# Optimization experiments

Measured on AMD Instinct MI355X. Metric: run time of the kernel, lower is better.

## Reference

```python
import jax, jax.numpy as jnp
import numpy as np

N_NODES = 50000
N_EDGES = 800000
F_IN = 64
F_HID = 64
K = 3


def _cheb_norm(edge_index, edge_weight, n):
    # PyG ChebConv sym normalization with lambda_max=2: Lhat = -D^{-1/2} A D^{-1/2}
    # (diagonal of Lhat is exactly 0, so self-loop terms vanish)
    row, col = edge_index[0], edge_index[1]
    deg = jax.ops.segment_sum(edge_weight, row, num_segments=n)
    dis = jnp.where(deg > 0, jax.lax.rsqrt(jnp.where(deg > 0, deg, 1.0)), 0.0)
    return -dis[row] * edge_weight * dis[col]


def _prop(x, row, col, norm, n):
    # out[i] = sum_{e: col[e]=i} norm[e] * x[row[e]]
    return jax.ops.segment_sum(x[row] * norm[:, None], col, num_segments=n)


def _cheb_conv(x, W, b, row, col, norm, n):
    # ChebConv K=3: Tx0=x, Tx1=Lhat x, Tx2=2 Lhat Tx1 - Tx0
    tx0 = x
    tx1 = _prop(x, row, col, norm, n)
    tx2 = 2.0 * _prop(tx1, row, col, norm, n) - tx0
    return tx0 @ W[0] + tx1 @ W[1] + tx2 @ W[2] + b


def setup_inputs() -> dict:
    key = jax.random.key(0)
    ks = jax.random.split(key, 20)
    inp = {
        "x": jax.random.normal(ks[0], (N_NODES, F_IN), dtype=jnp.float32),
        "edge_index": jax.random.randint(ks[1], (2, N_EDGES), 0, N_NODES, dtype=jnp.int32),
        "edge_weight": jax.random.uniform(ks[2], (N_EDGES,), dtype=jnp.float32),
    }
    # 6 ChebConvs: x->gate (F_IN->F_HID) and h->gate (F_HID->F_HID) for z, r, h
    names_in = [("Wxz", "bxz", F_IN), ("Whz", "bhz", F_HID), ("Wxr", "bxr", F_IN),
                ("Whr", "bhr", F_HID), ("Wxh", "bxh", F_IN), ("Whh", "bhh", F_HID)]
    for i, (wn, bn, fin) in enumerate(names_in):
        scale = 1.0 / np.sqrt(fin)
        inp[wn] = jax.random.normal(ks[3 + i], (K, fin, F_HID), dtype=jnp.float32) * scale
        inp[bn] = jnp.zeros((F_HID,), dtype=jnp.float32)
    inp["Wlin"] = jax.random.normal(ks[12], (F_HID, 2), dtype=jnp.float32) * (1.0 / np.sqrt(F_HID))
    inp["blin"] = jnp.zeros((2,), dtype=jnp.float32)
    return inp


def reference(x, edge_index, edge_weight, Wxz, bxz, Whz, bhz, Wxr, bxr, Whr, bhr,
              Wxh, bxh, Whh, bhh, Wlin, blin):
    n = x.shape[0]
    row, col = edge_index[0], edge_index[1]
    norm = _cheb_norm(edge_index, edge_weight, n)
    h0 = jnp.zeros((n, F_HID), dtype=x.dtype)
    # GConvGRU single step (initial hidden state = 0)
    z = jax.nn.sigmoid(_cheb_conv(x, Wxz, bxz, row, col, norm, n)
                       + _cheb_conv(h0, Whz, bhz, row, col, norm, n))
    r = jax.nn.sigmoid(_cheb_conv(x, Wxr, bxr, row, col, norm, n)
                       + _cheb_conv(h0, Whr, bhr, row, col, norm, n))
    h_tilde = jnp.tanh(_cheb_conv(x, Wxh, bxh, row, col, norm, n)
                       + _cheb_conv(h0 * r, Whh, bhh, row, col, norm, n))
    h = z * h0 + (1.0 - z) * h_tilde
    # head: dropout in eval mode (identity) -> tanh -> linear -> sigmoid
    return jax.nn.sigmoid(jnp.tanh(h) @ Wlin + blin)
```

## Files before the change

### kernel.cpp

```cpp
#include <hip/hip_runtime.h>
#include <hip/hip_bf16.h>

#define N_NODES 50000
#define N_EDGES 800000
#define NB1 400
#define CH  2000
#define NBKT 196
#define CAP 8192
#define SORT_MAX 6144

typedef unsigned short ushort_t;
typedef unsigned long long u64;
typedef __attribute__((ext_vector_type(8))) short bf16x8;
typedef __attribute__((ext_vector_type(4))) float f32x4;

constexpr int GCUR_O  = 0;
constexpr int DIS_O   = 512;
constexpr int OFF_O   = 50512;
constexpr int CSLOT_O = 100544;
constexpr int RSLOT_O = 3311808;
constexpr int RW_O    = 4917440;
constexpr int ABUF_O  = 6517440;
constexpr int PBUF_O  = 11317440;
constexpr int XS_O    = 11329728;
constexpr int T1S_O   = RSLOT_O;

__device__ __forceinline__ ushort_t f32_to_bf16(float f) {
    unsigned u = __float_as_uint(f);
    u += 0x7fffu + ((u >> 16) & 1u);
    return (ushort_t)(u >> 16);
}
__device__ __forceinline__ float bflo(unsigned u) { return __uint_as_float(u << 16); }
__device__ __forceinline__ float bfhi(unsigned u) { return __uint_as_float(u & 0xffff0000u); }
__device__ __forceinline__ unsigned packbf2(float a, float b) {
    return (unsigned)f32_to_bf16(a) | ((unsigned)f32_to_bf16(b) << 16);
}
__device__ __forceinline__ float fsigmoid(float x) { return 1.f / (1.f + __expf(-x)); }
__device__ __forceinline__ float ftanh(float x) {
    x = fminf(15.f, fmaxf(-15.f, x));
    float e = __expf(2.f * x);
    return (e - 1.f) / (e + 1.f);
}

__global__ __launch_bounds__(512) void k1(
    const int* __restrict__ ei, const float* __restrict__ ew,
    const float* __restrict__ x, const float* __restrict__ Wxz,
    const float* __restrict__ Wxh, unsigned* __restrict__ gcur,
    u64* __restrict__ cslot, unsigned* __restrict__ rslot,
    unsigned* __restrict__ abuf, ushort_t* __restrict__ pbuf) {
    int bid = blockIdx.x, t = threadIdx.x;
    if (bid < NB1) {
        __shared__ unsigned colbuf[CH], rowbuf[CH];
        __shared__ unsigned hc[256], hr[256], bc[256], br[256];
        if (t < 256) { hc[t] = 0; hr[t] = 0; }
        __syncthreads();
        int e0 = bid * CH;
        for (int i = t; i < CH; i += 512) {
            unsigned r = (unsigned)ei[e0 + i];
            unsigned c = (unsigned)ei[N_EDGES + e0 + i];
            rowbuf[i] = r;
            colbuf[i] = c;
            atomicAdd(&hc[c >> 8], 1u);
            atomicAdd(&hr[r >> 8], 1u);
        }
        __syncthreads();
        if (t < NBKT) {
            bc[t] = atomicAdd(&gcur[t], hc[t]);
            br[t] = atomicAdd(&gcur[256 + t], hr[t]);
        }
        __syncthreads();
        if (t < 256) { hc[t] = 0; hr[t] = 0; }
        __syncthreads();
        for (int i = t; i < CH; i += 512) {
            unsigned c = colbuf[i];
            unsigned r = rowbuf[i];
            unsigned w = __float_as_uint(ew[e0 + i]);
            unsigned dc = c >> 8;
            unsigned pc = bc[dc] + atomicAdd(&hc[dc], 1u);
            if (pc < CAP)
                cslot[dc * CAP + pc] = ((u64)w << 32) | ((c & 255u) << 16) | (r & 0xFFFFu);
            unsigned dr = r >> 8;
            unsigned pr = br[dr] + atomicAdd(&hr[dr], 1u);
            if (pr < CAP) rslot[dr * CAP + pr] = (w & 0xFFFFFF00u) | (r & 255u);
        }
    } else if (bid < NB1 + 98) {
        int n0 = (bid - NB1) * 512;
        for (int idx = t; idx < 512 * 32; idx += 512) {
            int n = n0 + (idx >> 5);
            if (n < N_NODES) {
                int q = idx & 31;
                float2 xv = ((const float2*)x)[n * 32 + q];
                abuf[n * 96 + q] = packbf2(xv.x, xv.y);
            }
        }
    } else {
        for (int idx = t; idx < 24576; idx += 512) {
            int k = idx >> 7, n = idx & 127;
            float v = (n < 64) ? Wxz[k * 64 + n] : Wxh[k * 64 + (n - 64)];
            int c = n >> 4, s = k >> 5, l = (((k >> 3) & 3) << 4) | (n & 15), j = k & 7;
            pbuf[((c * 6 + s) * 64 + l) * 8 + j] = f32_to_bf16(v);
        }
    }
}

__global__ __launch_bounds__(512) void k2(
    const float* __restrict__ x, const unsigned* __restrict__ gcur,
    const u64* __restrict__ cslot, const unsigned* __restrict__ rslot,
    float* __restrict__ dis, int* __restrict__ off,
    u64* __restrict__ rw, unsigned* __restrict__ xs) {
    int bid = blockIdx.x, t = threadIdx.x;
    __shared__ unsigned rawA[SORT_MAX], rawB[SORT_MAX];
    __shared__ unsigned hist[256], hsc[256], cur[256], gs[256];
    __shared__ float facc[256];

    if (bid < NBKT) {
        if (t < 256) {
            gs[t] = (t < NBKT) ? gcur[t] : 0u;
            hist[t] = 0;
        }
        __syncthreads();
        for (int o = 1; o < 256; o <<= 1) {
            unsigned v = (t < 256 && t >= o) ? gs[t - o] : 0u;
            __syncthreads();
            if (t < 256) gs[t] += v;
            __syncthreads();
        }
        unsigned szb = gcur[bid];
        unsigned sz = min(szb, (unsigned)SORT_MAX);
        unsigned base = gs[bid] - szb;
        for (unsigned i = t; i < sz; i += 512) {
            u64 v = cslot[bid * CAP + i];
            unsigned lo = (unsigned)v;
            rawA[i] = lo;
            rawB[i] = (unsigned)(v >> 32);
            atomicAdd(&hist[(lo >> 16) & 255u], 1u);
        }
        __syncthreads();
        unsigned h0 = (t < 256) ? hist[t] : 0u;
        if (t < 256) hsc[t] = h0;
        __syncthreads();
        for (int o = 1; o < 256; o <<= 1) {
            unsigned v = (t < 256 && t >= o) ? hsc[t - o] : 0u;
            __syncthreads();
            if (t < 256) hsc[t] += v;
            __syncthreads();
        }
        if (t < 256) {
            hsc[t] -= h0;
            cur[t] = 0u;
            int c = bid * 256 + t;
            if (c <= N_NODES) off[c] = (int)(base + hsc[t]);
        }
        __syncthreads();
        for (unsigned i = t; i < sz; i += 512) {
            unsigned lo = rawA[i];
            unsigned d = (lo >> 16) & 255u;
            unsigned p = hsc[d] + atomicAdd(&cur[d], 1u);
            rw[base + p] = ((u64)rawB[i] << 32) | (lo & 0xFFFFu);
        }
    } else {
        int b = bid - NBKT;
        if (t < 256) facc[t] = 0.f;
        __syncthreads();
        unsigned szr = min(gcur[256 + b], (unsigned)CAP);
        for (unsigned i = t; i < szr; i += 512) {
            unsigned v = rslot[b * CAP + i];
            atomicAdd(&facc[v & 255u], __uint_as_float(v & 0xFFFFFF00u));
        }
        __syncthreads();
        if (t < 256) {
            float d = facc[t];
            float r = d > 0.f ? rsqrtf(d) : 0.f;
            facc[t] = r;
            int n = b * 256 + t;
            if (n < N_NODES) dis[n] = r;
        }
        __syncthreads();
        for (int idx = t; idx < 8192; idx += 512) {
            int nl = idx >> 5, q = idx & 31;
            int n = b * 256 + nl;
            if (n < N_NODES) {
                float2 xv = ((const float2*)x)[n * 32 + q];
                float r = facc[nl];
                xs[n * 32 + q] = packbf2(r * xv.x, r * xv.y);
            }
        }
    }
}

__global__ __launch_bounds__(256) void k_prop(
    const int* __restrict__ off, const u64* __restrict__ rw,
    const unsigned* __restrict__ xsrc, const float* __restrict__ dis,
    const float* __restrict__ xf, unsigned* __restrict__ abuf,
    unsigned* __restrict__ t1s, int mode) {
    int node = (blockIdx.x * 256 + threadIdx.x) >> 6;
    if (node >= N_NODES) return;
    int lane = threadIdx.x & 63, h = lane >> 5, q = lane & 31;
    int b = off[node], end = off[node + 1];
    float di = dis[node];
    float acc0 = 0.f, acc1 = 0.f;
    for (; b + 7 < end; b += 8) {
        u64 v0 = rw[b + h], v1 = rw[b + h + 2], v2 = rw[b + h + 4], v3 = rw[b + h + 6];
        unsigned r0 = (unsigned)v0 & 0xFFFFu, r1 = (unsigned)v1 & 0xFFFFu;
        unsigned r2 = (unsigned)v2 & 0xFFFFu, r3 = (unsigned)v3 & 0xFFFFu;
        float a0 = __uint_as_float((unsigned)(v0 >> 32));
        float a1 = __uint_as_float((unsigned)(v1 >> 32));
        float a2 = __uint_as_float((unsigned)(v2 >> 32));
        float a3 = __uint_as_float((unsigned)(v3 >> 32));
        unsigned u0 = xsrc[r0 * 32 + q], u1 = xsrc[r1 * 32 + q];
        unsigned u2 = xsrc[r2 * 32 + q], u3 = xsrc[r3 * 32 + q];
        acc0 += a0 * bflo(u0) + a1 * bflo(u1) + a2 * bflo(u2) + a3 * bflo(u3);
        acc1 += a0 * bfhi(u0) + a1 * bfhi(u1) + a2 * bfhi(u2) + a3 * bfhi(u3);
    }
    for (; b + 1 < end; b += 2) {
        u64 v = rw[b + h];
        unsigned r = (unsigned)v & 0xFFFFu;
        float a = __uint_as_float((unsigned)(v >> 32));
        unsigned u = xsrc[r * 32 + q];
        acc0 += a * bflo(u); acc1 += a * bfhi(u);
    }
    if (b < end && h == 0) {
        u64 v = rw[b];
        unsigned r = (unsigned)v & 0xFFFFu;
        float a = __uint_as_float((unsigned)(v >> 32));
        unsigned u = xsrc[r * 32 + q];
        acc0 += a * bflo(u); acc1 += a * bfhi(u);
    }
    acc0 += __shfl_xor(acc0, 32, 64);
    acc1 += __shfl_xor(acc1, 32, 64);
    if (h == 0) {
        float t0 = -di * acc0, t1v = -di * acc1;
        if (mode == 0) {
            abuf[node * 96 + 32 + q] = packbf2(t0, t1v);
            t1s[node * 32 + q] = packbf2(di * t0, di * t1v);
        } else {
            float2 xv = ((const float2*)xf)[node * 32 + q];
            abuf[node * 96 + 64 + q] = packbf2(2.f * t0 - xv.x, 2.f * t1v - xv.y);
        }
    }
}

__global__ __launch_bounds__(256) void k_gemm(
    const ushort_t* __restrict__ ab, const ushort_t* __restrict__ pbuf,
    const float* __restrict__ bxz, const float* __restrict__ bhz,
    const float* __restrict__ bxh, const float* __restrict__ bhh,
    const float* __restrict__ Wlin, const float* __restrict__ blin,
    float2* __restrict__ out) {
    __shared__ ushort_t bsh[24576];
    int tid = threadIdx.x;
    {
        uint4* s4 = (uint4*)bsh;
        const uint4* g4 = (const uint4*)pbuf;
        for (int i = tid; i < 3072; i += 256) s4[i] = g4[i];
    }
    __syncthreads();

    int wave = tid >> 6, lane = tid & 63;
    int quad = lane >> 4, m = lane & 15;
    int arow = blockIdx.x * 64 + wave * 16 + m;
    const ushort_t* ap = ab + (size_t)arow * 192 + quad * 8;

    f32x4 acc[8];
#pragma unroll
    for (int c = 0; c < 8; ++c) acc[c] = (f32x4){0.f, 0.f, 0.f, 0.f};
#pragma unroll
    for (int s = 0; s < 6; ++s) {
        bf16x8 af = *(const bf16x8*)(ap + s * 32);
#pragma unroll
        for (int c = 0; c < 8; ++c) {
            bf16x8 bfr = *(const bf16x8*)(bsh + ((c * 6 + s) * 64 + lane) * 8);
            acc[c] = __builtin_amdgcn_mfma_f32_16x16x32_bf16(af, bfr, acc[c], 0, 0, 0);
        }
    }
    float bzv[4], bhv[4], wl0[4], wl1[4];
#pragma unroll
    for (int c = 0; c < 4; ++c) {
        int col = c * 16 + m;
        bzv[c] = bxz[col] + bhz[col];
        bhv[c] = bxh[col] + bhh[col];
        wl0[c] = Wlin[2 * col];
        wl1[c] = Wlin[2 * col + 1];
    }
    float bl0 = blin[0], bl1 = blin[1];
#pragma unroll
    for (int i = 0; i < 4; ++i) {
        float p0 = 0.f, p1 = 0.f;
#pragma unroll
        for (int c = 0; c < 4; ++c) {
            float z  = fsigmoid(acc[c][i] + bzv[c]);
            float ht = ftanh(acc[c + 4][i] + bhv[c]);
            float t  = ftanh((1.f - z) * ht);
            p0 += t * wl0[c];
            p1 += t * wl1[c];
        }
        for (int o = 1; o <= 8; o <<= 1) {
            p0 += __shfl_xor(p0, o, 64);
            p1 += __shfl_xor(p1, o, 64);
        }
        int g = blockIdx.x * 64 + wave * 16 + quad * 4 + i;
        if (m == 0 && g < N_NODES)
            out[g] = make_float2(fsigmoid(p0 + bl0), fsigmoid(p1 + bl1));
    }
}

extern "C" void kernel_launch(void* const* d_in, const int* in_sizes, int n_in,
                              void* d_out, int out_size, void* d_ws, size_t ws_size,
                              hipStream_t stream) {
    const float* x    = (const float*)d_in[0];
    const int*   ei   = (const int*)d_in[1];
    const float* ew   = (const float*)d_in[2];
    const float* Wxz  = (const float*)d_in[3];
    const float* bxz  = (const float*)d_in[4];
    const float* bhz  = (const float*)d_in[6];
    const float* Wxh  = (const float*)d_in[11];
    const float* bxh  = (const float*)d_in[12];
    const float* bhh  = (const float*)d_in[14];
    const float* Wlin = (const float*)d_in[15];
    const float* blin = (const float*)d_in[16];

    float*    ws    = (float*)d_ws;
    unsigned* gcur  = (unsigned*)(ws + GCUR_O);
    float*    dis   = ws + DIS_O;
    int*      off   = (int*)(ws + OFF_O);
    u64*      cslot = (u64*)(ws + CSLOT_O);
    unsigned* rslot = (unsigned*)(ws + RSLOT_O);
    u64*      rw    = (u64*)(ws + RW_O);
    unsigned* abuf  = (unsigned*)(ws + ABUF_O);
    ushort_t* pbuf  = (ushort_t*)(ws + PBUF_O);
    unsigned* xs    = (unsigned*)(ws + XS_O);
    unsigned* t1s   = (unsigned*)(ws + T1S_O);

    hipMemsetAsync(d_ws, 0, 512 * 4, stream);

    k1<<<NB1 + 98 + 1, 512, 0, stream>>>(ei, ew, x, Wxz, Wxh, gcur, cslot, rslot, abuf, pbuf);
    k2<<<NBKT * 2, 512, 0, stream>>>(x, gcur, cslot, rslot, dis, off, rw, xs);
    k_prop<<<12500, 256, 0, stream>>>(off, rw, xs, dis, x, abuf, t1s, 0);
    k_prop<<<12500, 256, 0, stream>>>(off, rw, t1s, dis, x, abuf, abuf, 1);
    k_gemm<<<782, 256, 0, stream>>>((const ushort_t*)abuf, pbuf, bxz, bhz, bxh, bhh,
                                    Wlin, blin, (float2*)d_out);
}
```

Before: 214.2 us.

## Fuse graph build, normalization and both propagations into one cooperative kernel

```diff
diff --git a/kernel.cpp b/kernel.cpp
--- a/kernel.cpp
+++ b/kernel.cpp
@@ -1,5 +1,7 @@
 #include <hip/hip_runtime.h>
 #include <hip/hip_bf16.h>
+#include <hip/hip_cooperative_groups.h>
+namespace cg = cooperative_groups;
 
 #define N_NODES 50000
 #define N_EDGES 800000
@@ -7,7 +9,7 @@
 #define CH  2000
 #define NBKT 196
 #define CAP 8192
-#define SORT_MAX 6144
+#define GRID_ALL 512
 
 typedef unsigned short ushort_t;
 typedef unsigned long long u64;
@@ -42,17 +44,25 @@
     return (e - 1.f) / (e + 1.f);
 }
 
-__global__ __launch_bounds__(512) void k1(
+__global__ __launch_bounds__(512, 4) void k_all(
     const int* __restrict__ ei, const float* __restrict__ ew,
     const float* __restrict__ x, const float* __restrict__ Wxz,
     const float* __restrict__ Wxh, unsigned* __restrict__ gcur,
     u64* __restrict__ cslot, unsigned* __restrict__ rslot,
-    unsigned* __restrict__ abuf, ushort_t* __restrict__ pbuf) {
-    int bid = blockIdx.x, t = threadIdx.x;
+    float* __restrict__ dis, int* __restrict__ off, u64* __restrict__ rw,
+    unsigned* __restrict__ abuf, ushort_t* __restrict__ pbuf,
+    unsigned* __restrict__ xs, unsigned* __restrict__ t1s) {
+    cg::grid_group grid = cg::this_grid();
+    const int bid = blockIdx.x, t = threadIdx.x;
+    __shared__ unsigned colbuf[CH], rowbuf[CH];
+    __shared__ unsigned h1[256], h2[256], b1[256], b2[256];
+    __shared__ float facc[256];
+
+    if (bid == 0) gcur[t] = 0u;
+    grid.sync();
+
     if (bid < NB1) {
-        __shared__ unsigned colbuf[CH], rowbuf[CH];
-        __shared__ unsigned hc[256], hr[256], bc[256], br[256];
-        if (t < 256) { hc[t] = 0; hr[t] = 0; }
+        if (t < 256) { h1[t] = 0; h2[t] = 0; }
         __syncthreads();
         int e0 = bid * CH;
         for (int i = t; i < CH; i += 512) {
@@ -60,27 +70,27 @@
             unsigned c = (unsigned)ei[N_EDGES + e0 + i];
             rowbuf[i] = r;
             colbuf[i] = c;
-            atomicAdd(&hc[c >> 8], 1u);
-            atomicAdd(&hr[r >> 8], 1u);
+            atomicAdd(&h1[c >> 8], 1u);
+            atomicAdd(&h2[r >> 8], 1u);
         }
         __syncthreads();
         if (t < NBKT) {
-            bc[t] = atomicAdd(&gcur[t], hc[t]);
-            br[t] = atomicAdd(&gcur[256 + t], hr[t]);
-        }
-        __syncthreads();
-        if (t < 256) { hc[t] = 0; hr[t] = 0; }
+            b1[t] = atomicAdd(&gcur[t], h1[t]);
+            b2[t] = atomicAdd(&gcur[256 + t], h2[t]);
+        }
+        __syncthreads();
+        if (t < 256) { h1[t] = 0; h2[t] = 0; }
         __syncthreads();
         for (int i = t; i < CH; i += 512) {
             unsigned c = colbuf[i];
             unsigned r = rowbuf[i];
             unsigned w = __float_as_uint(ew[e0 + i]);
             unsigned dc = c >> 8;
-            unsigned pc = bc[dc] + atomicAdd(&hc[dc], 1u);
+            unsigned pc = b1[dc] + atomicAdd(&h1[dc], 1u);
             if (pc < CAP)
                 cslot[dc * CAP + pc] = ((u64)w << 32) | ((c & 255u) << 16) | (r & 0xFFFFu);
             unsigned dr = r >> 8;
-            unsigned pr = br[dr] + atomicAdd(&hr[dr], 1u);
+            unsigned pr = b2[dr] + atomicAdd(&h2[dr], 1u);
             if (pr < CAP) rslot[dr * CAP + pr] = (w & 0xFFFFFF00u) | (r & 255u);
         }
     } else if (bid < NB1 + 98) {
@@ -93,7 +103,7 @@
                 abuf[n * 96 + q] = packbf2(xv.x, xv.y);
             }
         }
-    } else {
+    } else if (bid == NB1 + 98) {
         for (int idx = t; idx < 24576; idx += 512) {
             int k = idx >> 7, n = idx & 127;
             float v = (n < 64) ? Wxz[k * 64 + n] : Wxh[k * 64 + (n - 64)];
@@ -101,72 +111,58 @@
             pbuf[((c * 6 + s) * 64 + l) * 8 + j] = f32_to_bf16(v);
         }
     }
-}
-
-__global__ __launch_bounds__(512) void k2(
-    const float* __restrict__ x, const unsigned* __restrict__ gcur,
-    const u64* __restrict__ cslot, const unsigned* __restrict__ rslot,
-    float* __restrict__ dis, int* __restrict__ off,
-    u64* __restrict__ rw, unsigned* __restrict__ xs) {
-    int bid = blockIdx.x, t = threadIdx.x;
-    __shared__ unsigned rawA[SORT_MAX], rawB[SORT_MAX];
-    __shared__ unsigned hist[256], hsc[256], cur[256], gs[256];
-    __shared__ float facc[256];
+    grid.sync();
 
     if (bid < NBKT) {
         if (t < 256) {
-            gs[t] = (t < NBKT) ? gcur[t] : 0u;
-            hist[t] = 0;
+            b1[t] = (t < NBKT) ? gcur[t] : 0u;
+            h1[t] = 0;
         }
         __syncthreads();
         for (int o = 1; o < 256; o <<= 1) {
-            unsigned v = (t < 256 && t >= o) ? gs[t - o] : 0u;
+            unsigned v = (t < 256 && t >= o) ? b1[t - o] : 0u;
             __syncthreads();
-            if (t < 256) gs[t] += v;
+            if (t < 256) b1[t] += v;
             __syncthreads();
         }
         unsigned szb = gcur[bid];
-        unsigned sz = min(szb, (unsigned)SORT_MAX);
-        unsigned base = gs[bid] - szb;
+        unsigned sz = min(szb, (unsigned)CAP);
+        unsigned base = b1[bid] - szb;
+        const u64* cs = cslot + (size_t)bid * CAP;
+        for (unsigned i = t; i < sz; i += 512)
+            atomicAdd(&h1[((unsigned)cs[i] >> 16) & 255u], 1u);
+        __syncthreads();
+        unsigned h0 = (t < 256) ? h1[t] : 0u;
+        if (t < 256) h2[t] = h0;
+        __syncthreads();
+        for (int o = 1; o < 256; o <<= 1) {
+            unsigned v = (t < 256 && t >= o) ? h2[t - o] : 0u;
+            __syncthreads();
+            if (t < 256) h2[t] += v;
+            __syncthreads();
+        }
+        if (t < 256) {
+            h2[t] -= h0;
+            b2[t] = 0u;
+            int c = bid * 256 + t;
+            if (c <= N_NODES) off[c] = (int)(base + h2[t]);
+        }
+        __syncthreads();
         for (unsigned i = t; i < sz; i += 512) {
-            u64 v = cslot[bid * CAP + i];
+            u64 v = cs[i];
             unsigned lo = (unsigned)v;
-            rawA[i] = lo;
-            rawB[i] = (unsigned)(v >> 32);
-            atomicAdd(&hist[(lo >> 16) & 255u], 1u);
-        }
-        __syncthreads();
-        unsigned h0 = (t < 256) ? hist[t] : 0u;
-        if (t < 256) hsc[t] = h0;
-        __syncthreads();
-        for (int o = 1; o < 256; o <<= 1) {
-            unsigned v = (t < 256 && t >= o) ? hsc[t - o] : 0u;
-            __syncthreads();
-            if (t < 256) hsc[t] += v;
-            __syncthreads();
-        }
-        if (t < 256) {
-            hsc[t] -= h0;
-            cur[t] = 0u;
-            int c = bid * 256 + t;
-            if (c <= N_NODES) off[c] = (int)(base + hsc[t]);
-        }
-        __syncthreads();
-        for (unsigned i = t; i < sz; i += 512) {
-            unsigned lo = rawA[i];
             unsigned d = (lo >> 16) & 255u;
-            unsigned p = hsc[d] + atomicAdd(&cur[d], 1u);
-            rw[base + p] = ((u64)rawB[i] << 32) | (lo & 0xFFFFu);
-        }
-    } else {
+            unsigned p = h2[d] + atomicAdd(&b2[d], 1u);
+            rw[base + p] = ((v >> 32) << 32) | (lo & 0xFFFFu);
+        }
+    } else if (bid < 2 * NBKT) {
         int b = bid - NBKT;
         if (t < 256) facc[t] = 0.f;
         __syncthreads();
         unsigned szr = min(gcur[256 + b], (unsigned)CAP);
-        for (unsigned i = t; i < szr; i += 512) {
-            unsigned v = rslot[b * CAP + i];
-            atomicAdd(&facc[v & 255u], __uint_as_float(v & 0xFFFFFF00u));
-        }
+        const unsigned* rs = rslot + (size_t)b * CAP;
+        for (unsigned i = t; i < szr; i += 512)
+            atomicAdd(&facc[rs[i] & 255u], __uint_as_float(rs[i] & 0xFFFFFF00u));
         __syncthreads();
         if (t < 256) {
             float d = facc[t];
@@ -186,56 +182,70 @@
             }
         }
     }
-}
-
-__global__ __launch_bounds__(256) void k_prop(
-    const int* __restrict__ off, const u64* __restrict__ rw,
-    const unsigned* __restrict__ xsrc, const float* __restrict__ dis,
-    const float* __restrict__ xf, unsigned* __restrict__ abuf,
-    unsigned* __restrict__ t1s, int mode) {
-    int node = (blockIdx.x * 256 + threadIdx.x) >> 6;
-    if (node >= N_NODES) return;
-    int lane = threadIdx.x & 63, h = lane >> 5, q = lane & 31;
-    int b = off[node], end = off[node + 1];
-    float di = dis[node];
-    float acc0 = 0.f, acc1 = 0.f;
-    for (; b + 7 < end; b += 8) {
-        u64 v0 = rw[b + h], v1 = rw[b + h + 2], v2 = rw[b + h + 4], v3 = rw[b + h + 6];
-        unsigned r0 = (unsigned)v0 & 0xFFFFu, r1 = (unsigned)v1 & 0xFFFFu;
-        unsigned r2 = (unsigned)v2 & 0xFFFFu, r3 = (unsigned)v3 & 0xFFFFu;
-        float a0 = __uint_as_float((unsigned)(v0 >> 32));
-        float a1 = __uint_as_float((unsigned)(v1 >> 32));
-        float a2 = __uint_as_float((unsigned)(v2 >> 32));
-        float a3 = __uint_as_float((unsigned)(v3 >> 32));
-        unsigned u0 = xsrc[r0 * 32 + q], u1 = xsrc[r1 * 32 + q];
-        unsigned u2 = xsrc[r2 * 32 + q], u3 = xsrc[r3 * 32 + q];
-        acc0 += a0 * bflo(u0) + a1 * bflo(u1) + a2 * bflo(u2) + a3 * bflo(u3);
-        acc1 += a0 * bfhi(u0) + a1 * bfhi(u1) + a2 * bfhi(u2) + a3 * bfhi(u3);
-    }
-    for (; b + 1 < end; b += 2) {
-        u64 v = rw[b + h];
-        unsigned r = (unsigned)v & 0xFFFFu;
-        float a = __uint_as_float((unsigned)(v >> 32));
-        unsigned u = xsrc[r * 32 + q];
-        acc0 += a * bflo(u); acc1 += a * bfhi(u);
-    }
-    if (b < end && h == 0) {
-        u64 v = rw[b];
-        unsigned r = (unsigned)v & 0xFFFFu;
-        float a = __uint_as_float((unsigned)(v >> 32));
-        unsigned u = xsrc[r * 32 + q];
-        acc0 += a * bflo(u); acc1 += a * bfhi(u);
-    }
-    acc0 += __shfl_xor(acc0, 32, 64);
-    acc1 += __shfl_xor(acc1, 32, 64);
-    if (h == 0) {
-        float t0 = -di * acc0, t1v = -di * acc1;
-        if (mode == 0) {
+    grid.sync();
+
+    {
+        int hw = (bid * 512 + t) >> 5, q = t & 31;
+        for (int node = hw; node < N_NODES; node += GRID_ALL * 16) {
+            int b = off[node], end = off[node + 1];
+            float di = dis[node];
+            float a0 = 0.f, a1 = 0.f;
+            for (; b + 3 < end; b += 4) {
+                u64 v0 = rw[b], v1 = rw[b + 1], v2 = rw[b + 2], v3 = rw[b + 3];
+                unsigned u0 = xs[((unsigned)v0 & 0xFFFFu) * 32 + q];
+                unsigned u1 = xs[((unsigned)v1 & 0xFFFFu) * 32 + q];
+                unsigned u2 = xs[((unsigned)v2 & 0xFFFFu) * 32 + q];
+                unsigned u3 = xs[((unsigned)v3 & 0xFFFFu) * 32 + q];
+                float w0 = __uint_as_float((unsigned)(v0 >> 32));
+                float w1 = __uint_as_float((unsigned)(v1 >> 32));
+                float w2 = __uint_as_float((unsigned)(v2 >> 32));
+                float w3 = __uint_as_float((unsigned)(v3 >> 32));
+                a0 += w0 * bflo(u0) + w1 * bflo(u1) + w2 * bflo(u2) + w3 * bflo(u3);
+                a1 += w0 * bfhi(u0) + w1 * bfhi(u1) + w2 * bfhi(u2) + w3 * bfhi(u3);
+            }
+            for (; b < end; ++b) {
+                u64 v = rw[b];
+                unsigned u = xs[((unsigned)v & 0xFFFFu) * 32 + q];
+                float w = __uint_as_float((unsigned)(v >> 32));
+                a0 += w * bflo(u);
+                a1 += w * bfhi(u);
+            }
+            float t0 = -di * a0, t1v = -di * a1;
             abuf[node * 96 + 32 + q] = packbf2(t0, t1v);
             t1s[node * 32 + q] = packbf2(di * t0, di * t1v);
-        } else {
-            float2 xv = ((const float2*)xf)[node * 32 + q];
-            abuf[node * 96 + 64 + q] = packbf2(2.f * t0 - xv.x, 2.f * t1v - xv.y);
+        }
+    }
+    grid.sync();
+
+    {
+        int hw = (bid * 512 + t) >> 5, q = t & 31;
+        for (int node = hw; node < N_NODES; node += GRID_ALL * 16) {
+            int b = off[node], end = off[node + 1];
+            float di = dis[node];
+            float a0 = 0.f, a1 = 0.f;
+            for (; b + 3 < end; b += 4) {
+                u64 v0 = rw[b], v1 = rw[b + 1], v2 = rw[b + 2], v3 = rw[b + 3];
+                unsigned u0 = t1s[((unsigned)v0 & 0xFFFFu) * 32 + q];
+                unsigned u1 = t1s[((unsigned)v1 & 0xFFFFu) * 32 + q];
+                unsigned u2 = t1s[((unsigned)v2 & 0xFFFFu) * 32 + q];
+                unsigned u3 = t1s[((unsigned)v3 & 0xFFFFu) * 32 + q];
+                float w0 = __uint_as_float((unsigned)(v0 >> 32));
+                float w1 = __uint_as_float((unsigned)(v1 >> 32));
+                float w2 = __uint_as_float((unsigned)(v2 >> 32));
+                float w3 = __uint_as_float((unsigned)(v3 >> 32));
+                a0 += w0 * bflo(u0) + w1 * bflo(u1) + w2 * bflo(u2) + w3 * bflo(u3);
+                a1 += w0 * bfhi(u0) + w1 * bfhi(u1) + w2 * bfhi(u2) + w3 * bfhi(u3);
+            }
+            for (; b < end; ++b) {
+                u64 v = rw[b];
+                unsigned u = t1s[((unsigned)v & 0xFFFFu) * 32 + q];
+                float w = __uint_as_float((unsigned)(v >> 32));
+                a0 += w * bflo(u);
+                a1 += w * bfhi(u);
+            }
+            float2 xv = ((const float2*)x)[node * 32 + q];
+            abuf[node * 96 + 64 + q] = packbf2(-2.f * di * a0 - xv.x,
+                                               -2.f * di * a1 - xv.y);
         }
     }
 }
@@ -306,9 +316,9 @@
 extern "C" void kernel_launch(void* const* d_in, const int* in_sizes, int n_in,
                               void* d_out, int out_size, void* d_ws, size_t ws_size,
                               hipStream_t stream) {
-    const float* x    = (const float*)d_in[0];
     const int*   ei   = (const int*)d_in[1];
     const float* ew   = (const float*)d_in[2];
+    const float* x    = (const float*)d_in[0];
     const float* Wxz  = (const float*)d_in[3];
     const float* bxz  = (const float*)d_in[4];
     const float* bhz  = (const float*)d_in[6];
@@ -330,12 +340,12 @@
     unsigned* xs    = (unsigned*)(ws + XS_O);
     unsigned* t1s   = (unsigned*)(ws + T1S_O);
 
-    hipMemsetAsync(d_ws, 0, 512 * 4, stream);
-
-    k1<<<NB1 + 98 + 1, 512, 0, stream>>>(ei, ew, x, Wxz, Wxh, gcur, cslot, rslot, abuf, pbuf);
-    k2<<<NBKT * 2, 512, 0, stream>>>(x, gcur, cslot, rslot, dis, off, rw, xs);
-    k_prop<<<12500, 256, 0, stream>>>(off, rw, xs, dis, x, abuf, t1s, 0);
-    k_prop<<<12500, 256, 0, stream>>>(off, rw, t1s, dis, x, abuf, abuf, 1);
+    void* args[] = {(void*)&ei, (void*)&ew, (void*)&x, (void*)&Wxz, (void*)&Wxh,
+                    (void*)&gcur, (void*)&cslot, (void*)&rslot, (void*)&dis,
+                    (void*)&off, (void*)&rw, (void*)&abuf, (void*)&pbuf,
+                    (void*)&xs, (void*)&t1s};
+    hipLaunchCooperativeKernel((const void*)k_all, dim3(GRID_ALL), dim3(512),
+                               args, 0, stream);
     k_gemm<<<782, 256, 0, stream>>>((const ushort_t*)abuf, pbuf, bxz, bhz, bxh, bhh,
                                     Wlin, blin, (float2*)d_out);
 }
```

After: 478.4 us. 2.23x slower.

## Locally sort edges per block before scatter, move x bf16 packing into k2, widen gather unroll

Applied to the files above, without the earlier changes.

```diff
diff --git a/kernel.cpp b/kernel.cpp
--- a/kernel.cpp
+++ b/kernel.cpp
@@ -42,25 +42,28 @@
     return (e - 1.f) / (e + 1.f);
 }
 
-__global__ __launch_bounds__(512) void k1(
+__global__ __launch_bounds__(512, 4) void k1(
     const int* __restrict__ ei, const float* __restrict__ ew,
-    const float* __restrict__ x, const float* __restrict__ Wxz,
-    const float* __restrict__ Wxh, unsigned* __restrict__ gcur,
-    u64* __restrict__ cslot, unsigned* __restrict__ rslot,
-    unsigned* __restrict__ abuf, ushort_t* __restrict__ pbuf) {
+    const float* __restrict__ Wxz, const float* __restrict__ Wxh,
+    unsigned* __restrict__ gcur, u64* __restrict__ cslot,
+    unsigned* __restrict__ rslot, ushort_t* __restrict__ pbuf) {
     int bid = blockIdx.x, t = threadIdx.x;
+    __shared__ u64 pC[CH];
+    __shared__ u64 sC[CH];
+    __shared__ unsigned sR[CH];
+    __shared__ unsigned char dCp[CH], dRp[CH];
+    __shared__ unsigned hc[256], hr[256], scC[256], scR[256], bc[256], br[256];
     if (bid < NB1) {
-        __shared__ unsigned colbuf[CH], rowbuf[CH];
-        __shared__ unsigned hc[256], hr[256], bc[256], br[256];
         if (t < 256) { hc[t] = 0; hr[t] = 0; }
         __syncthreads();
         int e0 = bid * CH;
         for (int i = t; i < CH; i += 512) {
             unsigned r = (unsigned)ei[e0 + i];
             unsigned c = (unsigned)ei[N_EDGES + e0 + i];
-            rowbuf[i] = r;
-            colbuf[i] = c;
-            atomicAdd(&hc[c >> 8], 1u);
+            unsigned w = __float_as_uint(ew[e0 + i]);
+            unsigned dc = c >> 8;
+            pC[i] = ((u64)w << 32) | (dc << 24) | ((c & 255u) << 16) | (r & 0xFFFFu);
+            atomicAdd(&hc[dc], 1u);
             atomicAdd(&hr[r >> 8], 1u);
         }
         __syncthreads();
@@ -68,30 +71,39 @@
             bc[t] = atomicAdd(&gcur[t], hc[t]);
             br[t] = atomicAdd(&gcur[256 + t], hr[t]);
         }
-        __syncthreads();
-        if (t < 256) { hc[t] = 0; hr[t] = 0; }
+        unsigned vC = (t < 256) ? hc[t] : 0u, vR = (t < 256) ? hr[t] : 0u;
+        if (t < 256) { scC[t] = vC; scR[t] = vR; }
+        __syncthreads();
+        for (int o = 1; o < 256; o <<= 1) {
+            unsigned aC = (t < 256 && t >= o) ? scC[t - o] : 0u;
+            unsigned aR = (t < 256 && t >= o) ? scR[t - o] : 0u;
+            __syncthreads();
+            if (t < 256) { scC[t] += aC; scR[t] += aR; }
+            __syncthreads();
+        }
+        if (t < 256) { scC[t] -= vC; scR[t] -= vR; hc[t] = 0; hr[t] = 0; }
         __syncthreads();
         for (int i = t; i < CH; i += 512) {
-            unsigned c = colbuf[i];
-            unsigned r = rowbuf[i];
-            unsigned w = __float_as_uint(ew[e0 + i]);
-            unsigned dc = c >> 8;
-            unsigned pc = bc[dc] + atomicAdd(&hc[dc], 1u);
-            if (pc < CAP)
-                cslot[dc * CAP + pc] = ((u64)w << 32) | ((c & 255u) << 16) | (r & 0xFFFFu);
+            u64 p = pC[i];
+            unsigned dc = (unsigned)(p >> 24) & 255u;
+            unsigned pc = scC[dc] + atomicAdd(&hc[dc], 1u);
+            sC[pc] = p;
+            dCp[pc] = (unsigned char)dc;
+            unsigned r = (unsigned)p & 0xFFFFu;
+            unsigned w = (unsigned)(p >> 32);
             unsigned dr = r >> 8;
-            unsigned pr = br[dr] + atomicAdd(&hr[dr], 1u);
-            if (pr < CAP) rslot[dr * CAP + pr] = (w & 0xFFFFFF00u) | (r & 255u);
-        }
-    } else if (bid < NB1 + 98) {
-        int n0 = (bid - NB1) * 512;
-        for (int idx = t; idx < 512 * 32; idx += 512) {
-            int n = n0 + (idx >> 5);
-            if (n < N_NODES) {
-                int q = idx & 31;
-                float2 xv = ((const float2*)x)[n * 32 + q];
-                abuf[n * 96 + q] = packbf2(xv.x, xv.y);
-            }
+            unsigned pr = scR[dr] + atomicAdd(&hr[dr], 1u);
+            sR[pr] = (w & 0xFFFFFF00u) | (r & 255u);
+            dRp[pr] = (unsigned char)dr;
+        }
+        __syncthreads();
+        for (int i = t; i < CH; i += 512) {
+            unsigned dc = dCp[i];
+            unsigned slotC = bc[dc] + (unsigned)i - scC[dc];
+            if (slotC < CAP) cslot[(size_t)dc * CAP + slotC] = sC[i];
+            unsigned dr = dRp[i];
+            unsigned slotR = br[dr] + (unsigned)i - scR[dr];
+            if (slotR < CAP) rslot[(size_t)dr * CAP + slotR] = sR[i];
         }
     } else {
         for (int idx = t; idx < 24576; idx += 512) {
@@ -106,8 +118,8 @@
 __global__ __launch_bounds__(512) void k2(
     const float* __restrict__ x, const unsigned* __restrict__ gcur,
     const u64* __restrict__ cslot, const unsigned* __restrict__ rslot,
-    float* __restrict__ dis, int* __restrict__ off,
-    u64* __restrict__ rw, unsigned* __restrict__ xs) {
+    float* __restrict__ dis, int* __restrict__ off, u64* __restrict__ rw,
+    unsigned* __restrict__ abuf, unsigned* __restrict__ xs) {
     int bid = blockIdx.x, t = threadIdx.x;
     __shared__ unsigned rawA[SORT_MAX], rawB[SORT_MAX];
     __shared__ unsigned hist[256], hsc[256], cur[256], gs[256];
@@ -129,7 +141,7 @@
         unsigned sz = min(szb, (unsigned)SORT_MAX);
         unsigned base = gs[bid] - szb;
         for (unsigned i = t; i < sz; i += 512) {
-            u64 v = cslot[bid * CAP + i];
+            u64 v = cslot[(size_t)bid * CAP + i];
             unsigned lo = (unsigned)v;
             rawA[i] = lo;
             rawB[i] = (unsigned)(v >> 32);
@@ -163,10 +175,9 @@
         if (t < 256) facc[t] = 0.f;
         __syncthreads();
         unsigned szr = min(gcur[256 + b], (unsigned)CAP);
-        for (unsigned i = t; i < szr; i += 512) {
-            unsigned v = rslot[b * CAP + i];
-            atomicAdd(&facc[v & 255u], __uint_as_float(v & 0xFFFFFF00u));
-        }
+        const unsigned* rs = rslot + (size_t)b * CAP;
+        for (unsigned i = t; i < szr; i += 512)
+            atomicAdd(&facc[rs[i] & 255u], __uint_as_float(rs[i] & 0xFFFFFF00u));
         __syncthreads();
         if (t < 256) {
             float d = facc[t];
@@ -182,6 +193,7 @@
             if (n < N_NODES) {
                 float2 xv = ((const float2*)x)[n * 32 + q];
                 float r = facc[nl];
+                abuf[n * 96 + q] = packbf2(xv.x, xv.y);
                 xs[n * 32 + q] = packbf2(r * xv.x, r * xv.y);
             }
         }
@@ -199,32 +211,44 @@
     int b = off[node], end = off[node + 1];
     float di = dis[node];
     float acc0 = 0.f, acc1 = 0.f;
-    for (; b + 7 < end; b += 8) {
-        u64 v0 = rw[b + h], v1 = rw[b + h + 2], v2 = rw[b + h + 4], v3 = rw[b + h + 6];
-        unsigned r0 = (unsigned)v0 & 0xFFFFu, r1 = (unsigned)v1 & 0xFFFFu;
-        unsigned r2 = (unsigned)v2 & 0xFFFFu, r3 = (unsigned)v3 & 0xFFFFu;
-        float a0 = __uint_as_float((unsigned)(v0 >> 32));
-        float a1 = __uint_as_float((unsigned)(v1 >> 32));
-        float a2 = __uint_as_float((unsigned)(v2 >> 32));
-        float a3 = __uint_as_float((unsigned)(v3 >> 32));
-        unsigned u0 = xsrc[r0 * 32 + q], u1 = xsrc[r1 * 32 + q];
-        unsigned u2 = xsrc[r2 * 32 + q], u3 = xsrc[r3 * 32 + q];
-        acc0 += a0 * bflo(u0) + a1 * bflo(u1) + a2 * bflo(u2) + a3 * bflo(u3);
-        acc1 += a0 * bfhi(u0) + a1 * bfhi(u1) + a2 * bfhi(u2) + a3 * bfhi(u3);
+    for (; b + 15 < end; b += 16) {
+        const u64* p = rw + b + h * 8;
+        u64 v0 = p[0], v1 = p[1], v2 = p[2], v3 = p[3];
+        u64 v4 = p[4], v5 = p[5], v6 = p[6], v7 = p[7];
+        unsigned u0 = xsrc[((unsigned)v0 & 0xFFFFu) * 32 + q];
+        unsigned u1 = xsrc[((unsigned)v1 & 0xFFFFu) * 32 + q];
+        unsigned u2 = xsrc[((unsigned)v2 & 0xFFFFu) * 32 + q];
+        unsigned u3 = xsrc[((unsigned)v3 & 0xFFFFu) * 32 + q];
+        unsigned u4 = xsrc[((unsigned)v4 & 0xFFFFu) * 32 + q];
+        unsigned u5 = xsrc[((unsigned)v5 & 0xFFFFu) * 32 + q];
+        unsigned u6 = xsrc[((unsigned)v6 & 0xFFFFu) * 32 + q];
+        unsigned u7 = xsrc[((unsigned)v7 & 0xFFFFu) * 32 + q];
+        float w0 = __uint_as_float((unsigned)(v0 >> 32));
+        float w1 = __uint_as_float((unsigned)(v1 >> 32));
+        float w2 = __uint_as_float((unsigned)(v2 >> 32));
+        float w3 = __uint_as_float((unsigned)(v3 >> 32));
+        float w4 = __uint_as_float((unsigned)(v4 >> 32));
+        float w5 = __uint_as_float((unsigned)(v5 >> 32));
+        float w6 = __uint_as_float((unsigned)(v6 >> 32));
+        float w7 = __uint_as_float((unsigned)(v7 >> 32));
+        acc0 += w0 * bflo(u0) + w1 * bflo(u1) + w2 * bflo(u2) + w3 * bflo(u3)
+              + w4 * bflo(u4) + w5 * bflo(u5) + w6 * bflo(u6) + w7 * bflo(u7);
+        acc1 += w0 * bfhi(u0) + w1 * bfhi(u1) + w2 * bfhi(u2) + w3 * bfhi(u3)
+              + w4 * bfhi(u4) + w5 * bfhi(u5) + w6 * bfhi(u6) + w7 * bfhi(u7);
     }
     for (; b + 1 < end; b += 2) {
         u64 v = rw[b + h];
-        unsigned r = (unsigned)v & 0xFFFFu;
-        float a = __uint_as_float((unsigned)(v >> 32));
-        unsigned u = xsrc[r * 32 + q];
-        acc0 += a * bflo(u); acc1 += a * bfhi(u);
+        unsigned u = xsrc[((unsigned)v & 0xFFFFu) * 32 + q];
+        float w = __uint_as_float((unsigned)(v >> 32));
+        acc0 += w * bflo(u);
+        acc1 += w * bfhi(u);
     }
     if (b < end && h == 0) {
         u64 v = rw[b];
-        unsigned r = (unsigned)v & 0xFFFFu;
-        float a = __uint_as_float((unsigned)(v >> 32));
-        unsigned u = xsrc[r * 32 + q];
-        acc0 += a * bflo(u); acc1 += a * bfhi(u);
+        unsigned u = xsrc[((unsigned)v & 0xFFFFu) * 32 + q];
+        float w = __uint_as_float((unsigned)(v >> 32));
+        acc0 += w * bflo(u);
+        acc1 += w * bfhi(u);
     }
     acc0 += __shfl_xor(acc0, 32, 64);
     acc1 += __shfl_xor(acc1, 32, 64);
@@ -332,8 +356,8 @@
 
     hipMemsetAsync(d_ws, 0, 512 * 4, stream);
 
-    k1<<<NB1 + 98 + 1, 512, 0, stream>>>(ei, ew, x, Wxz, Wxh, gcur, cslot, rslot, abuf, pbuf);
-    k2<<<NBKT * 2, 512, 0, stream>>>(x, gcur, cslot, rslot, dis, off, rw, xs);
+    k1<<<NB1 + 1, 512, 0, stream>>>(ei, ew, Wxz, Wxh, gcur, cslot, rslot, pbuf);
+    k2<<<NBKT * 2, 512, 0, stream>>>(x, gcur, cslot, rslot, dis, off, rw, abuf, xs);
     k_prop<<<12500, 256, 0, stream>>>(off, rw, xs, dis, x, abuf, t1s, 0);
     k_prop<<<12500, 256, 0, stream>>>(off, rw, t1s, dis, x, abuf, abuf, 1);
     k_gemm<<<782, 256, 0, stream>>>((const ushort_t*)abuf, pbuf, bxz, bhz, bxh, bhh,
```

After: 218.1 us. No clear change (+1.8%).
